# Kernel tuning notes

Measured on AMD Instinct MI355X. Metric: run time of the kernel, lower is better.

## Reference

```python
import jax, jax.numpy as jnp
import numpy as np
import math

B, L = 32, 4096
INPUT_SIZE, QUERY_SIZE, VALUE_SIZE, H = 1024, 64, 256, 16
DV = INPUT_SIZE // H  # per-head value dim = 64


def setup_inputs() -> dict:
    key = jax.random.key(0)
    ks = jax.random.split(key, 7)
    s_q = 1.0 / math.sqrt(INPUT_SIZE)
    s_v = 1.0 / math.sqrt(VALUE_SIZE)
    return {
        "query": jax.random.normal(ks[0], (B, INPUT_SIZE), jnp.float32),
        "key": jax.random.normal(ks[1], (B, L, QUERY_SIZE), jnp.float32),
        "value": jax.random.normal(ks[2], (B, L, VALUE_SIZE), jnp.float32),
        # query_heads: Linear(input_size, head_num*query_size) with bias
        "Wq": jax.random.uniform(ks[3], (H * QUERY_SIZE, INPUT_SIZE), jnp.float32, -s_q, s_q),
        "bq": jax.random.uniform(ks[4], (H * QUERY_SIZE,), jnp.float32, -s_q, s_q),
        # value_proj: Linear(value_size, input_size) with bias (concatenate=True)
        "Wv": jax.random.uniform(ks[5], (INPUT_SIZE, VALUE_SIZE), jnp.float32, -s_v, s_v),
        "bv": jax.random.uniform(ks[6], (INPUT_SIZE,), jnp.float32, -s_v, s_v),
    }


def reference(query, key, value, Wq, bq, Wv, bv):
    # value projection: (B, L, input_size) -> (B, H, L, DV)
    v = jnp.einsum("bld,ed->ble", value, Wv) + bv
    v = v.reshape(B, L, H, DV).transpose(0, 2, 1, 3)
    # query projection: (B, input_size) -> (B, H, QUERY_SIZE)
    q = (query @ Wq.T + bq).reshape(B, H, QUERY_SIZE)
    # scores: (B, H, L); key shared across heads
    scores = jnp.einsum("bhd,bld->bhl", q, key) / math.sqrt(QUERY_SIZE)
    p = jax.nn.softmax(scores, axis=-1)
    # weighted sum: (B, H, DV) -> concat -> (B, input_size)
    out = jnp.einsum("bhl,bhld->bhd", p, v)
    return out.reshape(B, H * DV)
```

## Files before the change

kernel.cpp:

```cpp
#include <hip/hip_runtime.h>
#include <math.h>

#define B_   32
#define L_   4096
#define IN_  1024
#define QS_  64
#define VS_  256
#define H_   16
#define NCH_ 16
#define CL_  256

#define Q_OFF   0
#define M_OFF   32768
#define S_OFF   40960
#define CTX_OFF 49152

__device__ __forceinline__ float dot4(float4 a, float4 b) {
    return a.x*b.x + a.y*b.y + a.z*b.z + a.w*b.w;
}

__global__ __launch_bounds__(128) void qproj_kernel(
        const float* __restrict__ query, const float* __restrict__ Wq,
        const float* __restrict__ bq, float* __restrict__ ws) {
    const int t = threadIdx.x;
    const int c = blockIdx.x * 4 + (t >> 5);
    const int b = t & 31;
    const float4* wq4 = (const float4*)(Wq + (size_t)c * IN_);
    const float4* q4  = (const float4*)(query + (size_t)b * IN_);
    float4 acc = make_float4(0.f, 0.f, 0.f, 0.f);
    #pragma unroll 8
    for (int k = 0; k < IN_ / 4; ++k) {
        float4 w = wq4[k], q = q4[k];
        acc.x += w.x * q.x; acc.y += w.y * q.y;
        acc.z += w.z * q.z; acc.w += w.w * q.w;
    }
    float r = acc.x + acc.y + acc.z + acc.w + bq[c];
    ws[Q_OFF + b * 1024 + c] = r * 0.125f;
}

__global__ __launch_bounds__(256) void attn_chunk_kernel(
        const float* __restrict__ key, const float* __restrict__ value,
        float* __restrict__ ws) {
    __shared__ float4 qs4[256];
    __shared__ float4 ps4[CL_ * 4];
    __shared__ float  m_s[H_];
    __shared__ __align__(16) float scratch[8192];

    const int t  = threadIdx.x;
    const int ch = blockIdx.x, b = blockIdx.y;
    const int lm = t & 63, hq = t >> 6;
    const int l0 = ch * CL_;

    qs4[t] = ((const float4*)(ws + Q_OFF + (size_t)b * 1024))[t];
    __syncthreads();

    const float* keyb = key + ((size_t)b * L_ + l0) * QS_;
    float s[4][4];
    #pragma unroll
    for (int j = 0; j < 4; ++j)
        #pragma unroll
        for (int hh = 0; hh < 4; ++hh) s[j][hh] = 0.f;

    #pragma unroll
    for (int e4 = 0; e4 < 16; ++e4) {
        float4 qv[4];
        #pragma unroll
        for (int hh = 0; hh < 4; ++hh) qv[hh] = qs4[(hq * 4 + hh) * 16 + e4];
        #pragma unroll
        for (int j = 0; j < 4; ++j) {
            float4 kv = *(const float4*)(keyb + (size_t)(4 * lm + j) * QS_ + e4 * 4);
            #pragma unroll
            for (int hh = 0; hh < 4; ++hh) s[j][hh] += dot4(kv, qv[hh]);
        }
    }

    float* red = scratch;
    #pragma unroll
    for (int j = 0; j < 4; ++j)
        #pragma unroll
        for (int hh = 0; hh < 4; ++hh)
            red[(hq * 4 + hh) * 260 + 4 * lm + j] = s[j][hh];
    __syncthreads();

    float* m_ws = ws + M_OFF;
    #pragma unroll
    for (int r = 0; r < 4; ++r) {
        int h = hq * 4 + r;
        float v = red[h * 260 + lm];
        v = fmaxf(v, red[h * 260 + 64 + lm]);
        v = fmaxf(v, red[h * 260 + 128 + lm]);
        v = fmaxf(v, red[h * 260 + 192 + lm]);
        #pragma unroll
        for (int off = 32; off >= 1; off >>= 1) v = fmaxf(v, __shfl_xor(v, off));
        if (lm == 0) { m_s[h] = v; m_ws[(b * NCH_ + ch) * H_ + h] = v; }
    }
    __syncthreads();

    float p[4][4];
    #pragma unroll
    for (int j = 0; j < 4; ++j)
        #pragma unroll
        for (int hh = 0; hh < 4; ++hh)
            p[j][hh] = __expf(s[j][hh] - m_s[hq * 4 + hh]);
    #pragma unroll
    for (int j = 0; j < 4; ++j)
        ps4[(4 * lm + j) * 4 + hq] = make_float4(p[j][0], p[j][1], p[j][2], p[j][3]);
    #pragma unroll
    for (int j = 0; j < 4; ++j)
        #pragma unroll
        for (int hh = 0; hh < 4; ++hh)
            red[(hq * 4 + hh) * 260 + 4 * lm + j] = p[j][hh];
    __syncthreads();

    float* s_ws = ws + S_OFF;
    #pragma unroll
    for (int r = 0; r < 4; ++r) {
        int h = hq * 4 + r;
        float v = red[h * 260 + lm] + red[h * 260 + 64 + lm]
                + red[h * 260 + 128 + lm] + red[h * 260 + 192 + lm];
        #pragma unroll
        for (int off = 32; off >= 1; off >>= 1) v += __shfl_xor(v, off);
        if (lm == 0) s_ws[(b * NCH_ + ch) * H_ + h] = v;
    }

    float ctx[16][4];
    #pragma unroll
    for (int h = 0; h < 16; ++h)
        #pragma unroll
        for (int jj = 0; jj < 4; ++jj) ctx[h][jj] = 0.f;

    const float* valb = value + ((size_t)b * L_ + l0) * VS_;
    for (int i = 0; i < 64; ++i) {
        int l = hq * 64 + i;
        float4 v = *(const float4*)(valb + (size_t)l * VS_ + lm * 4);
        float4 pA = ps4[l * 4 + 0], pB = ps4[l * 4 + 1];
        float4 pC = ps4[l * 4 + 2], pD = ps4[l * 4 + 3];
        float pp[16] = {pA.x, pA.y, pA.z, pA.w, pB.x, pB.y, pB.z, pB.w,
                        pC.x, pC.y, pC.z, pC.w, pD.x, pD.y, pD.z, pD.w};
        #pragma unroll
        for (int h = 0; h < 16; ++h) {
            ctx[h][0] += pp[h] * v.x; ctx[h][1] += pp[h] * v.y;
            ctx[h][2] += pp[h] * v.z; ctx[h][3] += pp[h] * v.w;
        }
    }
    __syncthreads();

    float4* cb4 = (float4*)scratch;
    if (hq < 2) {
        #pragma unroll
        for (int h = 0; h < 16; ++h)
            cb4[(hq * 16 + h) * 64 + lm] =
                make_float4(ctx[h][0], ctx[h][1], ctx[h][2], ctx[h][3]);
    }
    __syncthreads();
    if (hq >= 2) {
        #pragma unroll
        for (int h = 0; h < 16; ++h) {
            float4 o = cb4[((hq - 2) * 16 + h) * 64 + lm];
            o.x += ctx[h][0]; o.y += ctx[h][1];
            o.z += ctx[h][2]; o.w += ctx[h][3];
            cb4[((hq - 2) * 16 + h) * 64 + lm] = o;
        }
    }
    __syncthreads();

    float* ctxw = ws + CTX_OFF + (size_t)(b * NCH_ + ch) * H_ * VS_;
    #pragma unroll
    for (int k = 0; k < 16; ++k) {
        int c = k * 256 + t;
        ctxw[c] = scratch[c] + scratch[4096 + c];
    }
}

__global__ __launch_bounds__(256) void reduce_proj_kernel(
        const float* __restrict__ Wv, const float* __restrict__ bv,
        const float* __restrict__ ws, float* __restrict__ out) {
    __shared__ __align__(16) float ctx_lds[VS_];
    const int t = threadIdx.x;
    const int b = blockIdx.x >> 4, h = blockIdx.x & 15;
    const float* m_ws   = ws + M_OFF;
    const float* s_ws   = ws + S_OFF;
    const float* ctx_ws = ws + CTX_OFF;

    float mc[16], wc[16];
    float M = -1e30f;
    #pragma unroll
    for (int c = 0; c < 16; ++c) {
        mc[c] = m_ws[(b * 16 + c) * 16 + h];
        M = fmaxf(M, mc[c]);
    }
    float S = 0.f;
    #pragma unroll
    for (int c = 0; c < 16; ++c) {
        float w = __expf(mc[c] - M);
        wc[c] = w;
        S += s_ws[(b * 16 + c) * 16 + h] * w;
    }
    const float inv = 1.f / S;

    float acc = 0.f;
    #pragma unroll
    for (int c = 0; c < 16; ++c)
        acc += wc[c] * ctx_ws[((size_t)(b * 16 + c) * 16 + h) * VS_ + t];
    ctx_lds[t] = acc * inv;
    __syncthreads();

    const int d = t >> 2, qq = t & 3;
    const float4* wv4 = (const float4*)(Wv + (size_t)(h * 64 + d) * VS_);
    const float4* cl4 = (const float4*)ctx_lds;
    float a = 0.f;
    #pragma unroll
    for (int i = 0; i < 16; ++i) a += dot4(wv4[qq * 16 + i], cl4[qq * 16 + i]);
    a += __shfl_xor(a, 1);
    a += __shfl_xor(a, 2);
    if (qq == 0) out[b * 1024 + h * 64 + d] = a + bv[h * 64 + d];
}

extern "C" void kernel_launch(void* const* d_in, const int* in_sizes, int n_in,
                              void* d_out, int out_size, void* d_ws, size_t ws_size,
                              hipStream_t stream) {
    (void)in_sizes; (void)n_in; (void)out_size; (void)ws_size;
    const float* query = (const float*)d_in[0];
    const float* key   = (const float*)d_in[1];
    const float* value = (const float*)d_in[2];
    const float* Wq    = (const float*)d_in[3];
    const float* bq    = (const float*)d_in[4];
    const float* Wv    = (const float*)d_in[5];
    const float* bv    = (const float*)d_in[6];
    float* out = (float*)d_out;
    float* ws  = (float*)d_ws;

    qproj_kernel<<<256, 128, 0, stream>>>(query, Wq, bq, ws);
    attn_chunk_kernel<<<dim3(NCH_, B_), 256, 0, stream>>>(key, value, ws);
    reduce_proj_kernel<<<B_ * H_, 256, 0, stream>>>(Wv, bv, ws, out);
}
```

Measured before the change: 292.5 us.

## Restructure attention chunks: per-wave heads, register softmax, smaller chunks, split-K qproj

Each wave in the attention kernel now owns 4 heads across the whole chunk. That lets the softmax max and sum reductions stay in registers through wave shuffles, and removes the big LDS scratch, the cross-wave context reduction and several barriers. Chunk length becomes a template parameter, and 128-row chunks (1024 blocks) are used when the workspace is large enough, which raises parallelism but doubles the context partials written to and read from global memory. The query projection splits the K dimension across 4 lanes and combines them with shuffles, which gives more threads and shorter dependency chains. The value loop is unrolled by 8 to batch the global loads.

```diff
diff --git a/kernel.cpp b/kernel.cpp
--- a/kernel.cpp
+++ b/kernel.cpp
@@ -7,57 +7,61 @@
 #define QS_  64
 #define VS_  256
 #define H_   16
-#define NCH_ 16
-#define CL_  256
-
-#define Q_OFF   0
-#define M_OFF   32768
-#define S_OFF   40960
-#define CTX_OFF 49152
+
+#define Q_OFF 0
+#define M_OFF 32768
 
 __device__ __forceinline__ float dot4(float4 a, float4 b) {
     return a.x*b.x + a.y*b.y + a.z*b.z + a.w*b.w;
 }
 
-__global__ __launch_bounds__(128) void qproj_kernel(
+__global__ __launch_bounds__(256) void qproj_kernel(
         const float* __restrict__ query, const float* __restrict__ Wq,
         const float* __restrict__ bq, float* __restrict__ ws) {
     const int t = threadIdx.x;
-    const int c = blockIdx.x * 4 + (t >> 5);
-    const int b = t & 31;
-    const float4* wq4 = (const float4*)(Wq + (size_t)c * IN_);
-    const float4* q4  = (const float4*)(query + (size_t)b * IN_);
+    const int g = blockIdx.x * 256 + t;
+    const int o = g >> 2, sub = g & 3;
+    const int b = o >> 10, c = o & 1023;
+
+    const float4* wq4 = (const float4*)(Wq + (size_t)c * IN_) + sub * 64;
+    const float4* q4  = (const float4*)(query + (size_t)b * IN_) + sub * 64;
     float4 acc = make_float4(0.f, 0.f, 0.f, 0.f);
     #pragma unroll 8
-    for (int k = 0; k < IN_ / 4; ++k) {
+    for (int k = 0; k < 64; ++k) {
         float4 w = wq4[k], q = q4[k];
         acc.x += w.x * q.x; acc.y += w.y * q.y;
         acc.z += w.z * q.z; acc.w += w.w * q.w;
     }
-    float r = acc.x + acc.y + acc.z + acc.w + bq[c];
-    ws[Q_OFF + b * 1024 + c] = r * 0.125f;
-}
-
-__global__ __launch_bounds__(256) void attn_chunk_kernel(
+    float r = acc.x + acc.y + acc.z + acc.w;
+    r += __shfl_xor(r, 1);
+    r += __shfl_xor(r, 2);
+    if (sub == 0) ws[Q_OFF + b * 1024 + c] = (r + bq[c]) * 0.125f;
+}
+
+template<int CL>
+__global__ __launch_bounds__(256, 4) void attn_chunk_kernel(
         const float* __restrict__ key, const float* __restrict__ value,
         float* __restrict__ ws) {
+    constexpr int NCH = L_ / CL;
+    constexpr int R   = CL / 64;
+    constexpr int S_OFF   = M_OFF + B_ * NCH * H_;
+    constexpr int CTX_OFF = S_OFF + B_ * NCH * H_;
+
     __shared__ float4 qs4[256];
-    __shared__ float4 ps4[CL_ * 4];
-    __shared__ float  m_s[H_];
-    __shared__ __align__(16) float scratch[8192];
+    __shared__ float4 ps4[4 * CL];
 
     const int t  = threadIdx.x;
     const int ch = blockIdx.x, b = blockIdx.y;
-    const int lm = t & 63, hq = t >> 6;
-    const int l0 = ch * CL_;
-
-    qs4[t] = ((const float4*)(ws + Q_OFF + (size_t)b * 1024))[t];
+    const int lm = t & 63, w = t >> 6;
+    const int l0 = ch * CL;
+
+    qs4[t] = ((const float4*)(ws + Q_OFF + (size_t)b * IN_))[t];
     __syncthreads();
 
     const float* keyb = key + ((size_t)b * L_ + l0) * QS_;
-    float s[4][4];
-    #pragma unroll
-    for (int j = 0; j < 4; ++j)
+    float s[R][4];
+    #pragma unroll
+    for (int j = 0; j < R; ++j)
         #pragma unroll
         for (int hh = 0; hh < 4; ++hh) s[j][hh] = 0.f;
 
@@ -65,144 +69,111 @@
     for (int e4 = 0; e4 < 16; ++e4) {
         float4 qv[4];
         #pragma unroll
-        for (int hh = 0; hh < 4; ++hh) qv[hh] = qs4[(hq * 4 + hh) * 16 + e4];
-        #pragma unroll
-        for (int j = 0; j < 4; ++j) {
-            float4 kv = *(const float4*)(keyb + (size_t)(4 * lm + j) * QS_ + e4 * 4);
+        for (int hh = 0; hh < 4; ++hh) qv[hh] = qs4[(4 * w + hh) * 16 + e4];
+        #pragma unroll
+        for (int j = 0; j < R; ++j) {
+            float4 kv = *(const float4*)(keyb + (size_t)(R * lm + j) * QS_ + e4 * 4);
             #pragma unroll
             for (int hh = 0; hh < 4; ++hh) s[j][hh] += dot4(kv, qv[hh]);
         }
     }
 
-    float* red = scratch;
-    #pragma unroll
-    for (int j = 0; j < 4; ++j)
-        #pragma unroll
-        for (int hh = 0; hh < 4; ++hh)
-            red[(hq * 4 + hh) * 260 + 4 * lm + j] = s[j][hh];
-    __syncthreads();
-
-    float* m_ws = ws + M_OFF;
-    #pragma unroll
-    for (int r = 0; r < 4; ++r) {
-        int h = hq * 4 + r;
-        float v = red[h * 260 + lm];
-        v = fmaxf(v, red[h * 260 + 64 + lm]);
-        v = fmaxf(v, red[h * 260 + 128 + lm]);
-        v = fmaxf(v, red[h * 260 + 192 + lm]);
+    float m[4];
+    #pragma unroll
+    for (int hh = 0; hh < 4; ++hh) {
+        float v = s[0][hh];
+        #pragma unroll
+        for (int j = 1; j < R; ++j) v = fmaxf(v, s[j][hh]);
         #pragma unroll
         for (int off = 32; off >= 1; off >>= 1) v = fmaxf(v, __shfl_xor(v, off));
-        if (lm == 0) { m_s[h] = v; m_ws[(b * NCH_ + ch) * H_ + h] = v; }
-    }
-    __syncthreads();
-
-    float p[4][4];
-    #pragma unroll
-    for (int j = 0; j < 4; ++j)
-        #pragma unroll
-        for (int hh = 0; hh < 4; ++hh)
-            p[j][hh] = __expf(s[j][hh] - m_s[hq * 4 + hh]);
-    #pragma unroll
-    for (int j = 0; j < 4; ++j)
-        ps4[(4 * lm + j) * 4 + hq] = make_float4(p[j][0], p[j][1], p[j][2], p[j][3]);
-    #pragma unroll
-    for (int j = 0; j < 4; ++j)
-        #pragma unroll
-        for (int hh = 0; hh < 4; ++hh)
-            red[(hq * 4 + hh) * 260 + 4 * lm + j] = p[j][hh];
-    __syncthreads();
-
-    float* s_ws = ws + S_OFF;
-    #pragma unroll
-    for (int r = 0; r < 4; ++r) {
-        int h = hq * 4 + r;
-        float v = red[h * 260 + lm] + red[h * 260 + 64 + lm]
-                + red[h * 260 + 128 + lm] + red[h * 260 + 192 + lm];
+        m[hh] = v;
+    }
+
+    float p[R][4];
+    #pragma unroll
+    for (int j = 0; j < R; ++j)
+        #pragma unroll
+        for (int hh = 0; hh < 4; ++hh) p[j][hh] = __expf(s[j][hh] - m[hh]);
+
+    float sum[4];
+    #pragma unroll
+    for (int hh = 0; hh < 4; ++hh) {
+        float v = p[0][hh];
+        #pragma unroll
+        for (int j = 1; j < R; ++j) v += p[j][hh];
         #pragma unroll
         for (int off = 32; off >= 1; off >>= 1) v += __shfl_xor(v, off);
-        if (lm == 0) s_ws[(b * NCH_ + ch) * H_ + h] = v;
-    }
-
-    float ctx[16][4];
-    #pragma unroll
-    for (int h = 0; h < 16; ++h)
-        #pragma unroll
-        for (int jj = 0; jj < 4; ++jj) ctx[h][jj] = 0.f;
-
-    const float* valb = value + ((size_t)b * L_ + l0) * VS_;
-    for (int i = 0; i < 64; ++i) {
-        int l = hq * 64 + i;
-        float4 v = *(const float4*)(valb + (size_t)l * VS_ + lm * 4);
-        float4 pA = ps4[l * 4 + 0], pB = ps4[l * 4 + 1];
-        float4 pC = ps4[l * 4 + 2], pD = ps4[l * 4 + 3];
-        float pp[16] = {pA.x, pA.y, pA.z, pA.w, pB.x, pB.y, pB.z, pB.w,
-                        pC.x, pC.y, pC.z, pC.w, pD.x, pD.y, pD.z, pD.w};
-        #pragma unroll
-        for (int h = 0; h < 16; ++h) {
-            ctx[h][0] += pp[h] * v.x; ctx[h][1] += pp[h] * v.y;
-            ctx[h][2] += pp[h] * v.z; ctx[h][3] += pp[h] * v.w;
+        sum[hh] = v;
+    }
+    if (lm == 0) {
+        #pragma unroll
+        for (int hh = 0; hh < 4; ++hh) {
+            ws[M_OFF + (b * NCH + ch) * H_ + 4 * w + hh] = m[hh];
+            ws[S_OFF + (b * NCH + ch) * H_ + 4 * w + hh] = sum[hh];
         }
     }
-    __syncthreads();
-
-    float4* cb4 = (float4*)scratch;
-    if (hq < 2) {
-        #pragma unroll
-        for (int h = 0; h < 16; ++h)
-            cb4[(hq * 16 + h) * 64 + lm] =
-                make_float4(ctx[h][0], ctx[h][1], ctx[h][2], ctx[h][3]);
-    }
-    __syncthreads();
-    if (hq >= 2) {
-        #pragma unroll
-        for (int h = 0; h < 16; ++h) {
-            float4 o = cb4[((hq - 2) * 16 + h) * 64 + lm];
-            o.x += ctx[h][0]; o.y += ctx[h][1];
-            o.z += ctx[h][2]; o.w += ctx[h][3];
-            cb4[((hq - 2) * 16 + h) * 64 + lm] = o;
+
+    #pragma unroll
+    for (int j = 0; j < R; ++j)
+        ps4[w * CL + R * lm + j] = make_float4(p[j][0], p[j][1], p[j][2], p[j][3]);
+
+    float4 ctx[4];
+    #pragma unroll
+    for (int hh = 0; hh < 4; ++hh) ctx[hh] = make_float4(0.f, 0.f, 0.f, 0.f);
+
+    const float*  valb = value + ((size_t)b * L_ + l0) * VS_;
+    const float4* psw  = ps4 + w * CL;
+    for (int i0 = 0; i0 < CL; i0 += 8) {
+        float4 vv[8], pv[8];
+        #pragma unroll
+        for (int u = 0; u < 8; ++u)
+            vv[u] = *(const float4*)(valb + (size_t)(i0 + u) * VS_ + 4 * lm);
+        #pragma unroll
+        for (int u = 0; u < 8; ++u) pv[u] = psw[i0 + u];
+        #pragma unroll
+        for (int u = 0; u < 8; ++u) {
+            const float* ph = (const float*)&pv[u];
+            #pragma unroll
+            for (int hh = 0; hh < 4; ++hh) {
+                ctx[hh].x += ph[hh] * vv[u].x;
+                ctx[hh].y += ph[hh] * vv[u].y;
+                ctx[hh].z += ph[hh] * vv[u].z;
+                ctx[hh].w += ph[hh] * vv[u].w;
+            }
         }
     }
-    __syncthreads();
-
-    float* ctxw = ws + CTX_OFF + (size_t)(b * NCH_ + ch) * H_ * VS_;
-    #pragma unroll
-    for (int k = 0; k < 16; ++k) {
-        int c = k * 256 + t;
-        ctxw[c] = scratch[c] + scratch[4096 + c];
-    }
-}
-
+
+    float* ctxw = ws + CTX_OFF + (size_t)((b * NCH + ch) * H_) * VS_;
+    #pragma unroll
+    for (int hh = 0; hh < 4; ++hh)
+        *(float4*)(ctxw + (size_t)(4 * w + hh) * VS_ + 4 * lm) = ctx[hh];
+}
+
+template<int CL>
 __global__ __launch_bounds__(256) void reduce_proj_kernel(
         const float* __restrict__ Wv, const float* __restrict__ bv,
         const float* __restrict__ ws, float* __restrict__ out) {
+    constexpr int NCH = L_ / CL;
+    constexpr int S_OFF   = M_OFF + B_ * NCH * H_;
+    constexpr int CTX_OFF = S_OFF + B_ * NCH * H_;
+
     __shared__ __align__(16) float ctx_lds[VS_];
     const int t = threadIdx.x;
     const int b = blockIdx.x >> 4, h = blockIdx.x & 15;
-    const float* m_ws   = ws + M_OFF;
-    const float* s_ws   = ws + S_OFF;
-    const float* ctx_ws = ws + CTX_OFF;
-
-    float mc[16], wc[16];
+
     float M = -1e30f;
     #pragma unroll
-    for (int c = 0; c < 16; ++c) {
-        mc[c] = m_ws[(b * 16 + c) * 16 + h];
-        M = fmaxf(M, mc[c]);
-    }
-    float S = 0.f;
-    #pragma unroll
-    for (int c = 0; c < 16; ++c) {
-        float w = __expf(mc[c] - M);
-        wc[c] = w;
-        S += s_ws[(b * 16 + c) * 16 + h] * w;
-    }
-    const float inv = 1.f / S;
-
-    float acc = 0.f;
-    #pragma unroll
-    for (int c = 0; c < 16; ++c)
-        acc += wc[c] * ctx_ws[((size_t)(b * 16 + c) * 16 + h) * VS_ + t];
-    ctx_lds[t] = acc * inv;
+    for (int c = 0; c < NCH; ++c)
+        M = fmaxf(M, ws[M_OFF + (b * NCH + c) * H_ + h]);
+
+    float S = 0.f, acc = 0.f;
+    #pragma unroll 4
+    for (int c = 0; c < NCH; ++c) {
+        float wgt = __expf(ws[M_OFF + (b * NCH + c) * H_ + h] - M);
+        S += ws[S_OFF + (b * NCH + c) * H_ + h] * wgt;
+        acc += wgt * ws[CTX_OFF + ((size_t)(b * NCH + c) * H_ + h) * VS_ + t];
+    }
+    ctx_lds[t] = acc / S;
     __syncthreads();
 
     const int d = t >> 2, qq = t & 3;
@@ -219,7 +190,7 @@
 extern "C" void kernel_launch(void* const* d_in, const int* in_sizes, int n_in,
                               void* d_out, int out_size, void* d_ws, size_t ws_size,
                               hipStream_t stream) {
-    (void)in_sizes; (void)n_in; (void)out_size; (void)ws_size;
+    (void)in_sizes; (void)n_in; (void)out_size;
     const float* query = (const float*)d_in[0];
     const float* key   = (const float*)d_in[1];
     const float* value = (const float*)d_in[2];
@@ -230,7 +201,14 @@
     float* out = (float*)d_out;
     float* ws  = (float*)d_ws;
 
-    qproj_kernel<<<256, 128, 0, stream>>>(query, Wq, bq, ws);
-    attn_chunk_kernel<<<dim3(NCH_, B_), 256, 0, stream>>>(key, value, ws);
-    reduce_proj_kernel<<<B_ * H_, 256, 0, stream>>>(Wv, bv, ws, out);
-}
+    qproj_kernel<<<512, 256, 0, stream>>>(query, Wq, bq, ws);
+
+    const size_t need128 = (size_t)(32768 + 2 * B_ * 32 * H_ + (size_t)B_ * 32 * H_ * VS_) * 4;
+    if (ws_size >= need128) {
+        attn_chunk_kernel<128><<<dim3(32, B_), 256, 0, stream>>>(key, value, ws);
+        reduce_proj_kernel<128><<<B_ * H_, 256, 0, stream>>>(Wv, bv, ws, out);
+    } else {
+        attn_chunk_kernel<256><<<dim3(16, B_), 256, 0, stream>>>(key, value, ws);
+        reduce_proj_kernel<256><<<B_ * H_, 256, 0, stream>>>(Wv, bv, ws, out);
+    }
+}
```

After: 289.2 us. About the same (-1.1%).
